# Kernel optimization log

Measured on AMD Instinct MI355X. Metric: run time of the kernel, lower is better.

The kernel has to match this reference:

```python
import jax, jax.numpy as jnp
import numpy as np

E = 1024      # embed_dim
QH = 16       # query heads
KVH = 4       # kv heads
HD = E // QH  # head_dim = 64
KVE = HD * KVH  # 256
EPS = 1e-5
ROPE_BASE = 10000.0


def rope(x, d):
    # Faithful to the source RoPE: d == number of heads (x.shape[-2]),
    # and the 'sequence' axis of the cache is x.shape[0] (the batch dim).
    # rope(x) = x*cos + (x*sin) * neg_half(x)  (note: nonlinear in x).
    b = x.shape[0]
    theta = 1.0 / (ROPE_BASE ** (jnp.arange(0, d, 2, dtype=jnp.float32) / d))  # (d//2,)
    seq_idx = jnp.arange(b, dtype=jnp.float32)                                 # (b,)
    idx_theta = seq_idx[:, None] * theta[None, :]                              # (b, d//2)
    idx2 = jnp.concatenate([idx_theta, idx_theta], axis=-1)                    # (b, d)
    # cached shape (b,1,1,d); source permutes (0,1,3,2) -> (b,1,d,1)
    cos = jnp.cos(idx2)[:, None, :, None]  # (b,1,d,1)
    sin = jnp.sin(idx2)[:, None, :, None]
    d2 = d // 2
    # split of the LAST dim (head_dim) at d//2 == num_heads//2, as in source
    neg = jnp.concatenate([-x[..., d2:], x[..., :d2]], axis=-1)
    return x * cos + (x * sin) * neg


def setup_inputs() -> dict:
    key = jax.random.key(0)
    ks = jax.random.split(key, 12)
    b, n = 1, 2048

    def xavier(k, shape):
        fan_out, fan_in = shape
        std = (2.0 / (fan_in + fan_out)) ** 0.5
        return jax.random.normal(k, shape, dtype=jnp.float32) * std

    return {
        "query": jax.random.normal(ks[0], (b, n, E), dtype=jnp.float32),
        "key": jax.random.normal(ks[1], (b, n, E), dtype=jnp.float32),
        "value": jax.random.normal(ks[2], (b, n, E), dtype=jnp.float32),
        "Wq": xavier(ks[3], (E, E)),
        "bq": jnp.zeros((E,), jnp.float32),
        "Wk": xavier(ks[4], (KVE, E)),
        "bk": jnp.zeros((KVE,), jnp.float32),
        "Wv": xavier(ks[5], (KVE, E)),
        "bv": jnp.zeros((KVE,), jnp.float32),
        "gamma": jnp.ones((E,), jnp.float32),
        "beta": jnp.zeros((E,), jnp.float32),
    }


def reference(query, key, value, Wq, bq, Wk, bk, Wv, bv, gamma, beta):
    b, n, _ = query.shape
    q = query @ Wq.T + bq            # (b,n,E)
    k = key @ Wk.T + bk              # (b,n,KVE)
    v = value @ Wv.T + bv            # (b,n,KVE)

    q = q.reshape(b, n, QH, HD)      # b n h d
    k = k.reshape(b, n, KVH, HD)
    v = v.reshape(b, n, KVH, HD)

    q = rope(q, QH)
    k = rope(k, KVH)

    # b n h d -> b h n d
    q = jnp.transpose(q, (0, 2, 1, 3))
    k = jnp.transpose(k, (0, 2, 1, 3))
    v = jnp.transpose(v, (0, 2, 1, 3))

    scale = float(HD) ** 0.5
    q = q / scale

    g = QH // KVH
    # 'b (h g) n d -> b g h n d' : h outer, g inner
    q = q.reshape(b, KVH, g, n, HD)              # (b, h, g, n, d)
    q = jnp.transpose(q, (0, 2, 1, 3, 4))        # (b, g, h, n, d)

    sim = jnp.einsum('bghnd,bhsd->bghns', q, k)  # (b,g,h,n,s)
    attn = jax.nn.softmax(sim, axis=-1)
    out = jnp.einsum('bghns,bhsd->bghnd', attn, v)

    # 'b g h n d -> b n (h g) d'
    out = jnp.transpose(out, (0, 3, 2, 1, 4))    # (b, n, h, g, d)
    x = out.reshape(b, n, QH * HD)               # (b, n, E)

    # LayerNorm (biased variance, as in torch)
    mu = jnp.mean(x, axis=-1, keepdims=True)
    var = jnp.mean((x - mu) ** 2, axis=-1, keepdims=True)
    x = (x - mu) * jax.lax.rsqrt(var + EPS) * gamma + beta

    # NOTE: source computes out_proj(x) but returns x, so out_proj is dead code.
    return x
```

## Files before the change

kernel.cpp:

```cpp
#include <hip/hip_runtime.h>
#include <math.h>

#define EDIM   1024
#define KVEDIM 256
#define HDIM   64
#define QHEADS 16

typedef __attribute__((ext_vector_type(8))) short short8;
typedef __attribute__((ext_vector_type(4))) float f32x4;

__device__ __forceinline__ unsigned pack2(float a, float b) {
    unsigned ua = __builtin_bit_cast(unsigned, a);
    unsigned ub = __builtin_bit_cast(unsigned, b);
    ua += 0x7fffu + ((ua >> 16) & 1u);
    ub += 0x7fffu + ((ub >> 16) & 1u);
    return (ua >> 16) | (ub & 0xffff0000u);
}
__device__ __forceinline__ short f2b(float a) {
    unsigned ua = __builtin_bit_cast(unsigned, a);
    ua += 0x7fffu + ((ua >> 16) & 1u);
    return (short)(ua >> 16);
}

__global__ __launch_bounds__(256)
void cvt_bf16(const float* __restrict__ s0, const float* __restrict__ s1,
              const float* __restrict__ s2, const float* __restrict__ s3,
              const float* __restrict__ s4, const float* __restrict__ s5,
              short* __restrict__ d0, short* __restrict__ d1,
              short* __restrict__ d2, short* __restrict__ d3,
              short* __restrict__ d4, short* __restrict__ d5,
              int n0, int n1, int n2, int n3, int n4, int n5)
{
    const float* s; short* d; int n;
    switch (blockIdx.y) {
        case 0: s = s0; d = d0; n = n0; break;
        case 1: s = s1; d = d1; n = n1; break;
        case 2: s = s2; d = d2; n = n2; break;
        case 3: s = s3; d = d3; n = n3; break;
        case 4: s = s4; d = d4; n = n4; break;
        default: s = s5; d = d5; n = n5; break;
    }
    int i = ((int)blockIdx.x * 256 + threadIdx.x) * 8;
    if (i >= n) return;
    float4 a = *(const float4*)&s[i];
    float4 b = *(const float4*)&s[i + 4];
    uint4 o;
    o.x = pack2(a.x, a.y); o.y = pack2(a.z, a.w);
    o.z = pack2(b.x, b.y); o.w = pack2(b.z, b.w);
    *(uint4*)&d[i] = o;
}

__global__ __launch_bounds__(256)
void proj_gemm(const short* __restrict__ Aq, const short* __restrict__ Ak,
               const short* __restrict__ Av,
               const short* __restrict__ Wqb, const short* __restrict__ Wkb,
               const short* __restrict__ Wvb,
               const float* __restrict__ bq, const float* __restrict__ bk,
               const float* __restrict__ bv,
               short* __restrict__ Cq, short* __restrict__ Ck,
               short* __restrict__ Cv, float qscale)
{
    const int bid = blockIdx.x;
    const short* A; const short* W; const float* bias; short* C;
    int N, bm, bn; float scale;
    if (bid < 128) {
        A = Aq; W = Wqb; bias = bq; C = Cq; N = EDIM; scale = qscale;
        bm = (bid >> 3) * 128; bn = (bid & 7) * 128;
    } else if (bid < 160) {
        int i = bid - 128;
        A = Ak; W = Wkb; bias = bk; C = Ck; N = KVEDIM; scale = 1.0f;
        bm = (i >> 1) * 128; bn = (i & 1) * 128;
    } else {
        int i = bid - 160;
        A = Av; W = Wvb; bias = bv; C = Cv; N = KVEDIM; scale = 1.0f;
        bm = (i >> 1) * 128; bn = (i & 1) * 128;
    }
    const int K = EDIM;

    __shared__ short As[128 * 72];
    __shared__ short Ws[128 * 72];

    const int t = threadIdx.x, lane = t & 63, wv = t >> 6;
    const int lm = lane & 15, quad = lane >> 4;
    const int q8 = quad * 8, q4 = quad * 4;
    const int wm = (wv & 1) * 64, wn = (wv >> 1) * 64;
    const int sr = t >> 3, sc = (t & 7) * 8;

    f32x4 zero = {0.f, 0.f, 0.f, 0.f};
    f32x4 acc[4][4];
    #pragma unroll
    for (int i = 0; i < 4; ++i)
        #pragma unroll
        for (int j = 0; j < 4; ++j) acc[i][j] = zero;

    for (int k0 = 0; k0 < K; k0 += 64) {
        __syncthreads();
        #pragma unroll
        for (int i = 0; i < 4; ++i) {
            int r = sr + i * 32;
            *(uint4*)&As[r * 72 + sc] = *(const uint4*)&A[(size_t)(bm + r) * K + k0 + sc];
            *(uint4*)&Ws[r * 72 + sc] = *(const uint4*)&W[(size_t)(bn + r) * K + k0 + sc];
        }
        __syncthreads();
        #pragma unroll
        for (int ks = 0; ks < 2; ++ks) {
            short8 af[4], bfr[4];
            #pragma unroll
            for (int i = 0; i < 4; ++i)
                af[i] = *(const short8*)&As[(wm + i * 16 + lm) * 72 + ks * 32 + q8];
            #pragma unroll
            for (int j = 0; j < 4; ++j)
                bfr[j] = *(const short8*)&Ws[(wn + j * 16 + lm) * 72 + ks * 32 + q8];
            #pragma unroll
            for (int i = 0; i < 4; ++i)
                #pragma unroll
                for (int j = 0; j < 4; ++j)
                    acc[i][j] = __builtin_amdgcn_mfma_f32_16x16x32_bf16(
                        af[i], bfr[j], acc[i][j], 0, 0, 0);
        }
    }

    #pragma unroll
    for (int j = 0; j < 4; ++j) {
        float bj = bias[bn + wn + j * 16 + lm];
        #pragma unroll
        for (int i = 0; i < 4; ++i)
            #pragma unroll
            for (int r = 0; r < 4; ++r)
                C[(size_t)(bm + wm + i * 16 + q4 + r) * N + bn + wn + j * 16 + lm] =
                    f2b((acc[i][j][r] + bj) * scale);
    }
}

__global__ __launch_bounds__(256)
void attn_mfma(const short* __restrict__ q, const short* __restrict__ k,
               const short* __restrict__ v, float* __restrict__ x, int n)
{
    __shared__ short Ks[64 * 72];
    __shared__ short Vt[64 * 72];
    __shared__ short Ps[64 * 72];
    __shared__ float Lred[4][64];

    const int qh = blockIdx.y, kvh = qh >> 2;
    const int r0 = blockIdx.x * 64;
    const int t = threadIdx.x;
    const int lane = t & 63, wv = t >> 6;
    const int lm = lane & 15, quad = lane >> 4;
    const int q8 = quad * 8, q4 = quad * 4;

    short8 qf[4][2];
    #pragma unroll
    for (int qt = 0; qt < 4; ++qt) {
        const short* qrow = &q[(size_t)(r0 + qt * 16 + lm) * EDIM + qh * HDIM];
        qf[qt][0] = *(const short8*)&qrow[q8];
        qf[qt][1] = *(const short8*)&qrow[32 + q8];
    }

    const int rt0 = (wv & 1) * 2;
    const int dt0 = (wv >> 1) * 2;

    f32x4 zero = {0.f, 0.f, 0.f, 0.f};
    f32x4 oacc[2][2];
    #pragma unroll
    for (int i = 0; i < 2; ++i)
        #pragma unroll
        for (int j = 0; j < 2; ++j) oacc[i][j] = zero;
    float lp[4] = {0.f, 0.f, 0.f, 0.f};

    const int krow = t >> 2, kc = (t & 3) * 8;
    const int vs4 = (t & 15) * 4, vd0 = (t >> 4) * 4;

    for (int s0 = 0; s0 < n; s0 += 64) {
        __syncthreads();
        {
            const uint4* ksrc = (const uint4*)&k[(size_t)(s0 + krow) * KVEDIM + kvh * HDIM];
            uint4 ka = ksrc[t & 3];
            uint4 kb = ksrc[(t & 3) + 4];
            *(uint4*)&Ks[krow * 72 + kc] = ka;
            *(uint4*)&Ks[krow * 72 + kc + 32] = kb;
        }
        {
            unsigned vr[4][2];
            #pragma unroll
            for (int i = 0; i < 4; ++i) {
                uint2 vv = *(const uint2*)&v[(size_t)(s0 + vs4 + i) * KVEDIM + kvh * HDIM + vd0];
                vr[i][0] = vv.x; vr[i][1] = vv.y;
            }
            #pragma unroll
            for (int j = 0; j < 4; ++j) {
                int w = j >> 1, hi = (j & 1) * 16;
                unsigned e0 = (vr[0][w] >> hi) & 0xffffu;
                unsigned e1 = (vr[1][w] >> hi) & 0xffffu;
                unsigned e2 = (vr[2][w] >> hi) & 0xffffu;
                unsigned e3 = (vr[3][w] >> hi) & 0xffffu;
                uint2 o; o.x = e0 | (e1 << 16); o.y = e2 | (e3 << 16);
                *(uint2*)&Vt[(vd0 + j) * 72 + vs4] = o;
            }
        }
        __syncthreads();

        short8 kf0 = *(const short8*)&Ks[(wv * 16 + lm) * 72 + q8];
        short8 kf1 = *(const short8*)&Ks[(wv * 16 + lm) * 72 + 32 + q8];
        #pragma unroll
        for (int qt = 0; qt < 4; ++qt) {
            f32x4 s = zero;
            s = __builtin_amdgcn_mfma_f32_16x16x32_bf16(kf0, qf[qt][0], s, 0, 0, 0);
            s = __builtin_amdgcn_mfma_f32_16x16x32_bf16(kf1, qf[qt][1], s, 0, 0, 0);
            float p0 = exp2f(s[0]);
            float p1 = exp2f(s[1]);
            float p2 = exp2f(s[2]);
            float p3 = exp2f(s[3]);
            lp[qt] += (p0 + p1) + (p2 + p3);
            uint2 pw; pw.x = pack2(p0, p1); pw.y = pack2(p2, p3);
            *(uint2*)&Ps[(qt * 16 + lm) * 72 + wv * 16 + q4] = pw;
        }
        __syncthreads();

        short8 vf[2][2];
        #pragma unroll
        for (int j = 0; j < 2; ++j) {
            vf[j][0] = *(const short8*)&Vt[((dt0 + j) * 16 + lm) * 72 + q8];
            vf[j][1] = *(const short8*)&Vt[((dt0 + j) * 16 + lm) * 72 + 32 + q8];
        }
        #pragma unroll
        for (int i = 0; i < 2; ++i) {
            short8 pf0 = *(const short8*)&Ps[((rt0 + i) * 16 + lm) * 72 + q8];
            short8 pf1 = *(const short8*)&Ps[((rt0 + i) * 16 + lm) * 72 + 32 + q8];
            #pragma unroll
            for (int j = 0; j < 2; ++j) {
                oacc[i][j] = __builtin_amdgcn_mfma_f32_16x16x32_bf16(pf0, vf[j][0], oacc[i][j], 0, 0, 0);
                oacc[i][j] = __builtin_amdgcn_mfma_f32_16x16x32_bf16(pf1, vf[j][1], oacc[i][j], 0, 0, 0);
            }
        }
    }

    #pragma unroll
    for (int qt = 0; qt < 4; ++qt) {
        float l = lp[qt];
        l += __shfl_xor(l, 16);
        l += __shfl_xor(l, 32);
        if (lane < 16) Lred[wv][qt * 16 + lm] = l;
    }
    __syncthreads();

    #pragma unroll
    for (int i = 0; i < 2; ++i) {
        #pragma unroll
        for (int r = 0; r < 4; ++r) {
            int row = (rt0 + i) * 16 + q4 + r;
            float lsum = (Lred[0][row] + Lred[1][row]) + (Lred[2][row] + Lred[3][row]);
            float inv = 1.0f / lsum;
            #pragma unroll
            for (int j = 0; j < 2; ++j)
                x[(size_t)(r0 + row) * EDIM + qh * HDIM + (dt0 + j) * 16 + lm] =
                    oacc[i][j][r] * inv;
        }
    }
}

__global__ __launch_bounds__(256)
void ln_kernel(float* __restrict__ x, const float* __restrict__ gamma,
               const float* __restrict__ beta)
{
    const int rowbase = (int)blockIdx.x * EDIM;
    const int t = threadIdx.x;

    float4 xv = *(const float4*)&x[rowbase + t * 4];
    float s  = xv.x + xv.y + xv.z + xv.w;
    float sq = xv.x * xv.x + xv.y * xv.y + xv.z * xv.z + xv.w * xv.w;
    #pragma unroll
    for (int m = 1; m < 64; m <<= 1) {
        s  += __shfl_xor(s,  m);
        sq += __shfl_xor(sq, m);
    }
    __shared__ float ws_[4], wq_[4];
    const int wave = t >> 6;
    if ((t & 63) == 0) { ws_[wave] = s; wq_[wave] = sq; }
    __syncthreads();
    s  = ws_[0] + ws_[1] + ws_[2] + ws_[3];
    sq = wq_[0] + wq_[1] + wq_[2] + wq_[3];

    const float mu   = s * (1.f / EDIM);
    const float var  = sq * (1.f / EDIM) - mu * mu;
    const float rstd = rsqrtf(var + 1e-5f);

    float4 g = *(const float4*)&gamma[t * 4];
    float4 b = *(const float4*)&beta[t * 4];
    float4 o;
    o.x = (xv.x - mu) * rstd * g.x + b.x;
    o.y = (xv.y - mu) * rstd * g.y + b.y;
    o.z = (xv.z - mu) * rstd * g.z + b.z;
    o.w = (xv.w - mu) * rstd * g.w + b.w;
    *(float4*)&x[rowbase + t * 4] = o;
}

extern "C" void kernel_launch(void* const* d_in, const int* in_sizes, int n_in,
                              void* d_out, int out_size, void* d_ws, size_t ws_size,
                              hipStream_t stream)
{
    const float* query = (const float*)d_in[0];
    const float* key   = (const float*)d_in[1];
    const float* value = (const float*)d_in[2];
    const float* Wq    = (const float*)d_in[3];
    const float* bq    = (const float*)d_in[4];
    const float* Wk    = (const float*)d_in[5];
    const float* bk    = (const float*)d_in[6];
    const float* Wv    = (const float*)d_in[7];
    const float* bv    = (const float*)d_in[8];
    const float* gamma = (const float*)d_in[9];
    const float* beta  = (const float*)d_in[10];
    float* out = (float*)d_out;

    const int n = in_sizes[0] / EDIM;

    short* qa  = (short*)d_ws;
    short* ka  = qa  + (size_t)n * EDIM;
    short* va  = ka  + (size_t)n * EDIM;
    short* wqb = va  + (size_t)n * EDIM;
    short* wkb = wqb + (size_t)EDIM * EDIM;
    short* wvb = wkb + (size_t)KVEDIM * EDIM;
    short* qb  = wvb + (size_t)KVEDIM * EDIM;
    short* kb  = qb  + (size_t)n * EDIM;
    short* vb  = kb  + (size_t)n * KVEDIM;

    const float qscale = 0.125f * 1.44269504088896f;

    cvt_bf16<<<dim3(1024, 6), 256, 0, stream>>>(
        query, key, value, Wq, Wk, Wv,
        qa, ka, va, wqb, wkb, wvb,
        n * EDIM, n * EDIM, n * EDIM, EDIM * EDIM, KVEDIM * EDIM, KVEDIM * EDIM);

    proj_gemm<<<dim3(192), 256, 0, stream>>>(
        qa, ka, va, wqb, wkb, wvb, bq, bk, bv, qb, kb, vb, qscale);

    attn_mfma<<<dim3(n / 64, QHEADS), 256, 0, stream>>>(qb, kb, vb, out, n);

    ln_kernel<<<dim3(n), 256, 0, stream>>>(out, gamma, beta);
}
```

Before: 178.1 us.

## Split attention over key blocks and merge partial sums in layernorm

Adds a split-K (flash-decoding style) split of the key sequence across a third grid dimension, up to 4-way when workspace allows. Each split writes unnormalized fp32 output partials and row sums, and the layernorm kernel adds them up and normalizes before computing statistics. This raises the block count above the original 512 (32x16) so the GPU is better occupied, at the cost of extra fp32 partial traffic. It also swaps the manual bf16 packing for v_cvt_pk_bf16_f32 and the V transpose shifts for perm instructions. No max subtraction is involved, so summing the partials stays exact.

```diff
diff --git a/kernel.cpp b/kernel.cpp
--- a/kernel.cpp
+++ b/kernel.cpp
@@ -20,6 +20,11 @@
     unsigned ua = __builtin_bit_cast(unsigned, a);
     ua += 0x7fffu + ((ua >> 16) & 1u);
     return (short)(ua >> 16);
+}
+__device__ __forceinline__ unsigned cvtpk(float a, float b) {
+    unsigned r;
+    asm("v_cvt_pk_bf16_f32 %0, %1, %2" : "=v"(r) : "v"(a), "v"(b));
+    return r;
 }
 
 __global__ __launch_bounds__(256)
@@ -134,7 +139,9 @@
 
 __global__ __launch_bounds__(256)
 void attn_mfma(const short* __restrict__ q, const short* __restrict__ k,
-               const short* __restrict__ v, float* __restrict__ x, int n)
+               const short* __restrict__ v, float* __restrict__ x,
+               float* __restrict__ opart, float* __restrict__ lpart,
+               int n, int s_len, int partial)
 {
     __shared__ short Ks[64 * 72];
     __shared__ short Vt[64 * 72];
@@ -170,7 +177,8 @@
     const int krow = t >> 2, kc = (t & 3) * 8;
     const int vs4 = (t & 15) * 4, vd0 = (t >> 4) * 4;
 
-    for (int s0 = 0; s0 < n; s0 += 64) {
+    const int s_lo = (int)blockIdx.z * s_len;
+    for (int s0 = s_lo; s0 < s_lo + s_len; s0 += 64) {
         __syncthreads();
         {
             const uint4* ksrc = (const uint4*)&k[(size_t)(s0 + krow) * KVEDIM + kvh * HDIM];
@@ -188,12 +196,11 @@
             }
             #pragma unroll
             for (int j = 0; j < 4; ++j) {
-                int w = j >> 1, hi = (j & 1) * 16;
-                unsigned e0 = (vr[0][w] >> hi) & 0xffffu;
-                unsigned e1 = (vr[1][w] >> hi) & 0xffffu;
-                unsigned e2 = (vr[2][w] >> hi) & 0xffffu;
-                unsigned e3 = (vr[3][w] >> hi) & 0xffffu;
-                uint2 o; o.x = e0 | (e1 << 16); o.y = e2 | (e3 << 16);
+                const unsigned sel = (j & 1) ? 0x07060302u : 0x05040100u;
+                const int w = j >> 1;
+                uint2 o;
+                o.x = __builtin_amdgcn_perm(vr[1][w], vr[0][w], sel);
+                o.y = __builtin_amdgcn_perm(vr[3][w], vr[2][w], sel);
                 *(uint2*)&Vt[(vd0 + j) * 72 + vs4] = o;
             }
         }
@@ -211,7 +218,7 @@
             float p2 = exp2f(s[2]);
             float p3 = exp2f(s[3]);
             lp[qt] += (p0 + p1) + (p2 + p3);
-            uint2 pw; pw.x = pack2(p0, p1); pw.y = pack2(p2, p3);
+            uint2 pw; pw.x = cvtpk(p0, p1); pw.y = cvtpk(p2, p3);
             *(uint2*)&Ps[(qt * 16 + lm) * 72 + wv * 16 + q4] = pw;
         }
         __syncthreads();
@@ -243,44 +250,80 @@
     }
     __syncthreads();
 
-    #pragma unroll
-    for (int i = 0; i < 2; ++i) {
-        #pragma unroll
-        for (int r = 0; r < 4; ++r) {
-            int row = (rt0 + i) * 16 + q4 + r;
-            float lsum = (Lred[0][row] + Lred[1][row]) + (Lred[2][row] + Lred[3][row]);
-            float inv = 1.0f / lsum;
-            #pragma unroll
-            for (int j = 0; j < 2; ++j)
-                x[(size_t)(r0 + row) * EDIM + qh * HDIM + (dt0 + j) * 16 + lm] =
-                    oacc[i][j][r] * inv;
+    if (partial) {
+        float* xp = opart + (size_t)blockIdx.z * n * EDIM;
+        #pragma unroll
+        for (int i = 0; i < 2; ++i) {
+            #pragma unroll
+            for (int r = 0; r < 4; ++r) {
+                int row = (rt0 + i) * 16 + q4 + r;
+                float lsum = (Lred[0][row] + Lred[1][row]) + (Lred[2][row] + Lred[3][row]);
+                if (dt0 == 0 && lm == 0)
+                    lpart[(size_t)blockIdx.z * n * QHEADS + (size_t)(r0 + row) * QHEADS + qh] = lsum;
+                #pragma unroll
+                for (int j = 0; j < 2; ++j)
+                    xp[(size_t)(r0 + row) * EDIM + qh * HDIM + (dt0 + j) * 16 + lm] =
+                        oacc[i][j][r];
+            }
+        }
+    } else {
+        #pragma unroll
+        for (int i = 0; i < 2; ++i) {
+            #pragma unroll
+            for (int r = 0; r < 4; ++r) {
+                int row = (rt0 + i) * 16 + q4 + r;
+                float lsum = (Lred[0][row] + Lred[1][row]) + (Lred[2][row] + Lred[3][row]);
+                float inv = 1.0f / lsum;
+                #pragma unroll
+                for (int j = 0; j < 2; ++j)
+                    x[(size_t)(r0 + row) * EDIM + qh * HDIM + (dt0 + j) * 16 + lm] =
+                        oacc[i][j][r] * inv;
+            }
         }
     }
 }
 
 __global__ __launch_bounds__(256)
 void ln_kernel(float* __restrict__ x, const float* __restrict__ gamma,
-               const float* __restrict__ beta)
-{
-    const int rowbase = (int)blockIdx.x * EDIM;
+               const float* __restrict__ beta,
+               const float* __restrict__ opart, const float* __restrict__ lpart,
+               int nsplit, int n)
+{
+    const int row = blockIdx.x;
     const int t = threadIdx.x;
 
-    float4 xv = *(const float4*)&x[rowbase + t * 4];
-    float s  = xv.x + xv.y + xv.z + xv.w;
+    float4 xv;
+    if (nsplit > 0) {
+        const int head = t >> 4;
+        float l = 0.f;
+        float4 s = {0.f, 0.f, 0.f, 0.f};
+        for (int z = 0; z < nsplit; ++z) {
+            const float4 o = *(const float4*)&opart[(size_t)z * n * EDIM +
+                                                    (size_t)row * EDIM + t * 4];
+            s.x += o.x; s.y += o.y; s.z += o.z; s.w += o.w;
+            l += lpart[(size_t)z * n * QHEADS + (size_t)row * QHEADS + head];
+        }
+        const float inv = 1.f / l;
+        xv.x = s.x * inv; xv.y = s.y * inv; xv.z = s.z * inv; xv.w = s.w * inv;
+    } else {
+        xv = *(const float4*)&x[(size_t)row * EDIM + t * 4];
+    }
+
+    float sm  = xv.x + xv.y + xv.z + xv.w;
     float sq = xv.x * xv.x + xv.y * xv.y + xv.z * xv.z + xv.w * xv.w;
     #pragma unroll
     for (int m = 1; m < 64; m <<= 1) {
-        s  += __shfl_xor(s,  m);
+        sm += __shfl_xor(sm, m);
         sq += __shfl_xor(sq, m);
     }
     __shared__ float ws_[4], wq_[4];
     const int wave = t >> 6;
-    if ((t & 63) == 0) { ws_[wave] = s; wq_[wave] = sq; }
+    if ((t & 63) == 0) { ws_[wave] = sm; wq_[wave] = sq; }
     __syncthreads();
-    s  = ws_[0] + ws_[1] + ws_[2] + ws_[3];
+    sm = ws_[0] + ws_[1] + ws_[2] + ws_[3];
     sq = wq_[0] + wq_[1] + wq_[2] + wq_[3];
 
-    const float mu   = s * (1.f / EDIM);
+    const float mu   = sm * (1.f / EDIM);
     const float var  = sq * (1.f / EDIM) - mu * mu;
     const float rstd = rsqrtf(var + 1e-5f);
 
@@ -291,7 +334,7 @@
     o.y = (xv.y - mu) * rstd * g.y + b.y;
     o.z = (xv.z - mu) * rstd * g.z + b.z;
     o.w = (xv.w - mu) * rstd * g.w + b.w;
-    *(float4*)&x[rowbase + t * 4] = o;
+    *(float4*)&x[(size_t)row * EDIM + t * 4] = o;
 }
 
 extern "C" void kernel_launch(void* const* d_in, const int* in_sizes, int n_in,
@@ -322,6 +365,18 @@
     short* qb  = wvb + (size_t)KVEDIM * EDIM;
     short* kb  = qb  + (size_t)n * EDIM;
     short* vb  = kb  + (size_t)n * KVEDIM;
+    short* ws_end = vb + (size_t)n * KVEDIM;
+
+    const size_t base_bytes = (size_t)((char*)ws_end - (char*)d_ws);
+    int nsplit = 0;
+    for (int cand = 4; cand >= 1; cand >>= 1) {
+        if (n % (64 * cand)) continue;
+        size_t need = base_bytes +
+                      (size_t)cand * ((size_t)n * EDIM + (size_t)n * QHEADS) * sizeof(float);
+        if (need <= ws_size) { nsplit = cand; break; }
+    }
+    float* opart = (float*)ws_end;
+    float* lpart = opart + (size_t)(nsplit > 0 ? nsplit : 1) * n * EDIM;
 
     const float qscale = 0.125f * 1.44269504088896f;
 
@@ -333,7 +388,10 @@
     proj_gemm<<<dim3(192), 256, 0, stream>>>(
         qa, ka, va, wqb, wkb, wvb, bq, bk, bv, qb, kb, vb, qscale);
 
-    attn_mfma<<<dim3(n / 64, QHEADS), 256, 0, stream>>>(qb, kb, vb, out, n);
-
-    ln_kernel<<<dim3(n), 256, 0, stream>>>(out, gamma, beta);
-}
+    const int zdim  = (nsplit > 0) ? nsplit : 1;
+    const int s_len = n / zdim;
+    attn_mfma<<<dim3(n / 64, QHEADS, zdim), 256, 0, stream>>>(
+        qb, kb, vb, out, opart, lpart, n, s_len, nsplit > 0 ? 1 : 0);
+
+    ln_kernel<<<dim3(n), 256, 0, stream>>>(out, gamma, beta, opart, lpart, nsplit, n);
+}
```

New measurement: 173.4 us. -2.6%, faster.
